# Kernel optimization log

Hardware: AMD Instinct MI355X
Metric: run time of the kernel (lower is better)

## Reference

```python
import jax, jax.numpy as jnp
import numpy as np

B, S, D = 8, 1024, 2048          # batch, seq_len, model dim (q_features == kv_features)
H, HD = 16, 128                   # num_heads, head_dim; H*HD == hidden == 2048


def setup_inputs() -> dict:
    key = jax.random.key(0)
    ks = jax.random.split(key, 6)
    fan_in = 1.0 / np.sqrt(D)     # variance_scaling(1.0, 'fan_in') style init scale
    return {
        "inputs_q": jax.random.normal(ks[0], (B, S, D), jnp.float32),
        "inputs_kv": jax.random.normal(ks[1], (B, S, D), jnp.float32),
        "Wq": jax.random.normal(ks[2], (D, H * HD), jnp.float32) * fan_in,
        "Wk": jax.random.normal(ks[3], (D, H * HD), jnp.float32) * fan_in,
        "Wv": jax.random.normal(ks[4], (D, H * HD), jnp.float32) * fan_in,
        "Wo": jax.random.normal(ks[5], (H * HD, D), jnp.float32) * (1.0 / np.sqrt(H * HD)),
    }


def reference(inputs_q, inputs_kv, Wq, Wk, Wv, Wo):
    b, sq, _ = inputs_q.shape
    skv = inputs_kv.shape[1]
    # QKV projections (DenseGeneral, no bias), reshape to heads
    # scale_attn_logits=True -> query scaled by 1/sqrt(head_dim)
    q = (inputs_q @ Wq).reshape(b, sq, H, HD) * (1.0 / np.sqrt(HD))
    k = (inputs_kv @ Wk).reshape(b, skv, H, HD)
    v = (inputs_kv @ Wv).reshape(b, skv, H, HD)
    # dot-product attention core: [b, h, q, k] scores -> softmax -> context
    scores = jnp.einsum('bqhd,bkhd->bhqk', q, k)
    attn = jax.nn.softmax(scores, axis=-1)
    ctx = jnp.einsum('bhqk,bkhd->bqhd', attn, v).reshape(b, sq, H * HD)
    # output projection back to q_features
    return ctx @ Wo
```

## Files before the change

kernel.cpp:

```cpp
#include <hip/hip_runtime.h>
#include <cstdint>
#include <cstddef>

#define B_  8
#define S_  1024
#define D_  2048
#define H_  16
#define HD_ 128
#define NT_ (D_ / 64)

typedef __bf16 bf16x8 __attribute__((ext_vector_type(8)));
typedef float  f32x4  __attribute__((ext_vector_type(4)));

__device__ __forceinline__ unsigned short f2b(float f) {
    unsigned int u = __float_as_uint(f);
    unsigned int r = (u + 0x7fffu + ((u >> 16) & 1u)) >> 16;
    return (unsigned short)r;
}

__device__ __forceinline__ void gl2lds16(const void* g, void* l) {
    __builtin_amdgcn_global_load_lds(
        (const __attribute__((address_space(1))) void*)g,
        (__attribute__((address_space(3))) void*)l, 16, 0, 0);
}

__global__ void cvt_f32_bf16(const float* __restrict__ src,
                             unsigned short* __restrict__ dst, int n4) {
    int i = blockIdx.x * blockDim.x + threadIdx.x;
    if (i >= n4) return;
    float4 v = ((const float4*)src)[i];
    ushort4 o;
    o.x = f2b(v.x); o.y = f2b(v.y); o.z = f2b(v.z); o.w = f2b(v.w);
    ((ushort4*)dst)[i] = o;
}

__global__ void wtrans(const float* __restrict__ W, unsigned short* __restrict__ Wt) {
    __shared__ float tile[32][33];
    int bx = blockIdx.x, by = blockIdx.y;
    int tx = threadIdx.x, ty = threadIdx.y;
#pragma unroll
    for (int i = 0; i < 4; i++)
        tile[ty + i * 8][tx] = W[(size_t)(by * 32 + ty + i * 8) * D_ + bx * 32 + tx];
    __syncthreads();
#pragma unroll
    for (int i = 0; i < 4; i++)
        Wt[(size_t)(bx * 32 + ty + i * 8) * D_ + by * 32 + tx] = f2b(tile[tx][ty + i * 8]);
}

__global__ void vtrans(const unsigned short* __restrict__ V, unsigned short* __restrict__ Vt) {
    __shared__ unsigned short tile[32][33];
    int bh = blockIdx.z;
    int b = bh >> 4, h = bh & 15;
    int tx = threadIdx.x, ty = threadIdx.y;
    int s0 = blockIdx.x * 32, hd0 = blockIdx.y * 32;
#pragma unroll
    for (int i = 0; i < 4; i++)
        tile[ty + i * 8][tx] = V[(size_t)(b * S_ + s0 + ty + i * 8) * D_ + h * HD_ + hd0 + tx];
    __syncthreads();
#pragma unroll
    for (int i = 0; i < 4; i++)
        Vt[((size_t)bh * HD_ + hd0 + ty + i * 8) * S_ + s0 + tx] = tile[tx][ty + i * 8];
}

#define STAGE1(TN, KH, SRC, DST) do {                                              \
    const int _kb = (TN) * 64 + (KH) * 32;                                         \
    _Pragma("unroll")                                                              \
    for (int _p = 0; _p < 2; _p++) {                                               \
        int _c = _p * 512 + tid;                                                   \
        int _row = _c >> 2;                                                        \
        int _j = (_c & 3) ^ ((_row >> 1) & 3);                                     \
        gl2lds16(SRC + (size_t)_row * D_ + _kb + _j * 8, DST + _c * 8);            \
    }                                                                              \
} while (0)

#define PHASE(SAP, SBP, MH, READB, TN, KH2, SSRC, SDST, VM) do {                   \
    asm volatile("" ::: "memory");                                                 \
    if (READB) {                                                                   \
        _Pragma("unroll")                                                          \
        for (int j = 0; j < 4; j++)                                                \
            bF[j] = *(const bf16x8*)(SAP##_unused, &SBP[(wn + j * 16 + l15) * 32 + swz]); \
    }                                                                              \
    bf16x8 aF[4];                                                                  \
    _Pragma("unroll")                                                              \
    for (int i = 0; i < 4; i++)                                                    \
        aF[i] = *(const bf16x8*)(&SAP[(wm + (MH) * 64 + i * 16 + l15) * 32 + swz]);\
    STAGE1(TN, KH2, SSRC, SDST);                                                   \
    asm volatile("" ::: "memory");                                                 \
    __builtin_amdgcn_s_barrier();                                                  \
    asm volatile("s_waitcnt lgkmcnt(0)" ::: "memory");                             \
    __builtin_amdgcn_sched_barrier(0);                                             \
    __builtin_amdgcn_s_setprio(1);                                                 \
    _Pragma("unroll")                                                              \
    for (int i = 0; i < 4; i++)                                                    \
        _Pragma("unroll")                                                          \
        for (int j = 0; j < 4; j++)                                                \
            acc[(MH) * 4 + i][j] =                                                 \
                __builtin_amdgcn_mfma_f32_16x16x32_bf16(aF[i], bF[j],              \
                                                        acc[(MH) * 4 + i][j], 0, 0, 0); \
    __builtin_amdgcn_s_setprio(0);                                                 \
    if (VM) asm volatile("s_waitcnt vmcnt(4)" ::: "memory");                       \
    asm volatile("" ::: "memory");                                                 \
    __builtin_amdgcn_s_barrier();                                                  \
} while (0)

#define sA00_unused 0
#define sA01_unused 0
#define sA10_unused 0
#define sA11_unused 0

template <bool OUTF>
__global__ void __launch_bounds__(512, 2)
gemm_bt3(const unsigned short* __restrict__ A0, const unsigned short* __restrict__ A1,
         const unsigned short* __restrict__ A2,
         const unsigned short* __restrict__ B0, const unsigned short* __restrict__ B1,
         const unsigned short* __restrict__ B2,
         unsigned short* __restrict__ o0, unsigned short* __restrict__ o1,
         unsigned short* __restrict__ o2, float* __restrict__ oF,
         float s0, float s1, float s2) {
    __shared__ __align__(16) unsigned short sA00[256 * 32], sA01[256 * 32];
    __shared__ __align__(16) unsigned short sA10[256 * 32], sA11[256 * 32];
    __shared__ __align__(16) unsigned short sB00[256 * 32], sB01[256 * 32];
    __shared__ __align__(16) unsigned short sB10[256 * 32], sB11[256 * 32];

    const int tid = threadIdx.x;
    const int w = tid >> 6, lane = tid & 63;
    const int l15 = lane & 15, lhi = lane >> 4;

    const int nwgx = gridDim.x;
    const int nwg = nwgx * gridDim.y;
    const int lin = blockIdx.y * nwgx + blockIdx.x;
    const int per = nwg >> 3;
    const int sw = (lin & 7) * per + (lin >> 3);
    const int bx = sw % nwgx, by = sw / nwgx;

    const int region = bx >> 3;
    const unsigned short* A  = region == 0 ? A0 : (region == 1 ? A1 : A2);
    const unsigned short* Bt = region == 0 ? B0 : (region == 1 ? B1 : B2);
    unsigned short* outB     = region == 0 ? o0 : (region == 1 ? o1 : o2);
    const float scale        = region == 0 ? s0 : (region == 1 ? s1 : s2);
    const int mBase = by * 256;
    const int nBase = (bx & 7) * 256;
    const int wm = (w >> 2) * 128, wn = (w & 3) * 64;

    const unsigned short* Ap = A  + (size_t)mBase * D_;
    const unsigned short* Bp = Bt + (size_t)nBase * D_;

    const int swz = (lhi ^ ((l15 >> 1) & 3)) * 8;

    f32x4 acc[8][4] = {};
    bf16x8 bF[4];

    STAGE1(0, 0, Ap, sA00);
    STAGE1(0, 0, Bp, sB00);
    STAGE1(0, 1, Ap, sA01);
    STAGE1(0, 1, Bp, sB01);
    asm volatile("s_waitcnt vmcnt(4)" ::: "memory");
    asm volatile("" ::: "memory");
    __builtin_amdgcn_s_barrier();

#pragma unroll 1
    for (int tt = 0; tt < NT_; tt += 2) {
        const int t1 = tt + 1;
        const int t2 = (tt + 2) & (NT_ - 1);
        PHASE(sA00, sB00, 0, true , t1, 0, Ap, sA10, false);
        PHASE(sA00, sB00, 1, false, t1, 0, Bp, sB10, true );
        PHASE(sA01, sB01, 0, true , t1, 1, Ap, sA11, false);
        PHASE(sA01, sB01, 1, false, t1, 1, Bp, sB11, true );
        PHASE(sA10, sB10, 0, true , t2, 0, Ap, sA00, false);
        PHASE(sA10, sB10, 1, false, t2, 0, Bp, sB00, true );
        PHASE(sA11, sB11, 0, true , t2, 1, Ap, sA01, false);
        PHASE(sA11, sB11, 1, false, t2, 1, Bp, sB01, true );
    }

#pragma unroll
    for (int ai = 0; ai < 8; ai++) {
#pragma unroll
        for (int j = 0; j < 4; j++) {
#pragma unroll
            for (int r = 0; r < 4; r++) {
                int row = mBase + wm + ai * 16 + lhi * 4 + r;
                int col = nBase + wn + j * 16 + l15;
                float v = acc[ai][j][r] * scale;
                if (OUTF) oF[(size_t)row * D_ + col] = v;
                else      outB[(size_t)row * D_ + col] = f2b(v);
            }
        }
    }
}

#define PSTR 72
__global__ void __launch_bounds__(256, 2)
attn(const unsigned short* __restrict__ Q,
     const unsigned short* __restrict__ Kb,
     const unsigned short* __restrict__ Vt,
     unsigned short* __restrict__ ctx) {
    __shared__ unsigned short sK[64 * 128];
    __shared__ unsigned short sV[128 * 64];
    __shared__ unsigned short sP[4 * 32 * PSTR];
    const int tid = threadIdx.x;
    const int w = tid >> 6, lane = tid & 63;
    const int l15 = lane & 15, lhi = lane >> 4;
    const int qt = blockIdx.x, h = blockIdx.y, b = blockIdx.z;
    const unsigned short* Qp = Q  + (size_t)b * S_ * D_ + h * HD_;
    const unsigned short* Kp = Kb + (size_t)b * S_ * D_ + h * HD_;
    const unsigned short* Vp = Vt + (size_t)(b * H_ + h) * HD_ * S_;
    const int q0 = qt * 128 + w * 32;

    int xoff[2];
#pragma unroll
    for (int ks = 0; ks < 2; ks++)
        xoff[ks] = (((ks * 4 + lhi) ^ (l15 & 7)) * 8);

    bf16x8 qF[2][4];
#pragma unroll
    for (int i = 0; i < 2; i++)
#pragma unroll
        for (int kk = 0; kk < 4; kk++)
            qF[i][kk] = *(const bf16x8*)(Qp + (size_t)(q0 + i * 16 + l15) * D_ + kk * 32 + lhi * 8);

    f32x4 o4[2][8] = {};
    float lrun[2][4] = {};
    unsigned short* sPw = sP + w * 32 * PSTR;

    for (int kt = 0; kt < S_ / 64; kt++) {
        __syncthreads();
#pragma unroll
        for (int p = 0; p < 4; p++) {
            int c = p * 256 + tid;
            {
                int row = c >> 4, pc = c & 15;
                int j = pc ^ (row & 7);
                gl2lds16(Kp + (size_t)(kt * 64 + row) * D_ + j * 8, sK + c * 8);
            }
            {
                int row = c >> 3, pc = c & 7;
                int j = pc ^ (row & 7);
                gl2lds16(Vp + (size_t)row * S_ + kt * 64 + j * 8, sV + c * 8);
            }
        }
        __syncthreads();

        f32x4 s4[2][4] = {};
#pragma unroll
        for (int j = 0; j < 4; j++) {
#pragma unroll
            for (int kk = 0; kk < 4; kk++) {
                bf16x8 bFk = *(const bf16x8*)(sK + (j * 16 + l15) * 128 + ((kk * 4 + lhi) ^ (l15 & 7)) * 8);
#pragma unroll
                for (int i = 0; i < 2; i++)
                    s4[i][j] = __builtin_amdgcn_mfma_f32_16x16x32_bf16(qF[i][kk], bFk, s4[i][j], 0, 0, 0);
            }
        }

#pragma unroll
        for (int i = 0; i < 2; i++) {
#pragma unroll
            for (int r = 0; r < 4; r++) {
                int prow = i * 16 + lhi * 4 + r;
                float ps = 0.f;
#pragma unroll
                for (int j = 0; j < 4; j++) {
                    float pv = exp2f(s4[i][j][r]);
                    ps += pv;
                    sPw[prow * PSTR + j * 16 + l15] = f2b(pv);
                }
                lrun[i][r] += ps;
            }
        }

#pragma unroll
        for (int k2 = 0; k2 < 2; k2++) {
            bf16x8 pF[2];
#pragma unroll
            for (int i = 0; i < 2; i++)
                pF[i] = *(const bf16x8*)(sPw + (i * 16 + l15) * PSTR + k2 * 32 + lhi * 8);
#pragma unroll
            for (int nt = 0; nt < 8; nt++) {
                bf16x8 vF = *(const bf16x8*)(sV + (nt * 16 + l15) * 64 + xoff[k2]);
#pragma unroll
                for (int i = 0; i < 2; i++)
                    o4[i][nt] = __builtin_amdgcn_mfma_f32_16x16x32_bf16(pF[i], vF, o4[i][nt], 0, 0, 0);
            }
        }
    }

#pragma unroll
    for (int i = 0; i < 2; i++)
#pragma unroll
        for (int r = 0; r < 4; r++) {
            float s = lrun[i][r];
#pragma unroll
            for (int msk = 1; msk < 16; msk <<= 1) s += __shfl_xor(s, msk);
            lrun[i][r] = 1.0f / s;
        }
#pragma unroll
    for (int i = 0; i < 2; i++)
#pragma unroll
        for (int nt = 0; nt < 8; nt++)
#pragma unroll
            for (int r = 0; r < 4; r++) {
                size_t row = (size_t)b * S_ + q0 + i * 16 + lhi * 4 + r;
                ctx[row * D_ + h * HD_ + nt * 16 + l15] = f2b(o4[i][nt][r] * lrun[i][r]);
            }
}

extern "C" void kernel_launch(void* const* d_in, const int* in_sizes, int n_in,
                              void* d_out, int out_size, void* d_ws, size_t ws_size,
                              hipStream_t stream) {
    const float* Xq  = (const float*)d_in[0];
    const float* Xkv = (const float*)d_in[1];
    const float* Wq  = (const float*)d_in[2];
    const float* Wk  = (const float*)d_in[3];
    const float* Wv  = (const float*)d_in[4];
    const float* Wo  = (const float*)d_in[5];
    float* out = (float*)d_out;

    char* ws = (char*)d_ws;
    const size_t XSZ = (size_t)B_ * S_ * D_ * 2;
    const size_t WSZ = (size_t)D_ * D_ * 2;
    unsigned short* XqB  = (unsigned short*)(ws);
    unsigned short* XkvB = (unsigned short*)(ws + XSZ);
    unsigned short* WqT  = (unsigned short*)(ws + 2 * XSZ);
    unsigned short* WkT  = (unsigned short*)(ws + 2 * XSZ + WSZ);
    unsigned short* WvT  = (unsigned short*)(ws + 2 * XSZ + 2 * WSZ);
    unsigned short* WoT  = (unsigned short*)(ws + 2 * XSZ + 3 * WSZ);
    unsigned short* Qb   = (unsigned short*)(ws + 3 * XSZ);
    unsigned short* Kb   = (unsigned short*)(ws + 4 * XSZ);
    unsigned short* Vb   = (unsigned short*)(ws + 5 * XSZ);
    unsigned short* VtB  = XkvB;
    unsigned short* ctxB = XqB;

    const int n4 = B_ * S_ * D_ / 4;
    cvt_f32_bf16<<<n4 / 256, 256, 0, stream>>>(Xq,  XqB,  n4);
    cvt_f32_bf16<<<n4 / 256, 256, 0, stream>>>(Xkv, XkvB, n4);

    dim3 tb(32, 8);
    wtrans<<<dim3(64, 64), tb, 0, stream>>>(Wq, WqT);
    wtrans<<<dim3(64, 64), tb, 0, stream>>>(Wk, WkT);
    wtrans<<<dim3(64, 64), tb, 0, stream>>>(Wv, WvT);
    wtrans<<<dim3(64, 64), tb, 0, stream>>>(Wo, WoT);

    const float qscale = 1.44269504088896f / 11.313708498984761f;

    gemm_bt3<false><<<dim3(24, 32), 512, 0, stream>>>(
        XqB, XkvB, XkvB, WqT, WkT, WvT, Qb, Kb, Vb, nullptr, qscale, 1.0f, 1.0f);

    vtrans<<<dim3(S_ / 32, HD_ / 32, B_ * H_), tb, 0, stream>>>(Vb, VtB);

    attn<<<dim3(S_ / 128, H_, B_), 256, 0, stream>>>(Qb, Kb, VtB, ctxB);

    gemm_bt3<true><<<dim3(8, 32), 512, 0, stream>>>(
        ctxB, ctxB, ctxB, WoT, WoT, WoT, nullptr, nullptr, nullptr, out, 1.0f, 1.0f, 1.0f);
}
```

Before: 638.0 us.

## Restructure GEMM mainloop as four-stage ring of 32-wide K tiles

Measured after the change: 639.4 us. Within noise of the previous version (+0.2%).

```diff
diff --git a/kernel.cpp b/kernel.cpp
--- a/kernel.cpp
+++ b/kernel.cpp
@@ -7,7 +7,7 @@
 #define D_  2048
 #define H_  16
 #define HD_ 128
-#define NT_ (D_ / 64)
+#define NT32_ 64
 
 typedef __bf16 bf16x8 __attribute__((ext_vector_type(8)));
 typedef float  f32x4  __attribute__((ext_vector_type(4)));
@@ -62,65 +62,67 @@
         Vt[((size_t)bh * HD_ + hd0 + ty + i * 8) * S_ + s0 + tx] = tile[tx][ty + i * 8];
 }
 
-#define STAGE1(TN, KH, SRC, DST) do {                                              \
-    const int _kb = (TN) * 64 + (KH) * 32;                                         \
+#define STAGE(TS, SRC, DST) do {                                                   \
+    const int _kb = (TS) * 32;                                                     \
     _Pragma("unroll")                                                              \
     for (int _p = 0; _p < 2; _p++) {                                               \
         int _c = _p * 512 + tid;                                                   \
         int _row = _c >> 2;                                                        \
-        int _j = (_c & 3) ^ ((_row >> 1) & 3);                                     \
+        int _j = (_c & 3) ^ (_row & 3);                                            \
         gl2lds16(SRC + (size_t)_row * D_ + _kb + _j * 8, DST + _c * 8);            \
     }                                                                              \
 } while (0)
 
-#define PHASE(SAP, SBP, MH, READB, TN, KH2, SSRC, SDST, VM) do {                   \
-    asm volatile("" ::: "memory");                                                 \
-    if (READB) {                                                                   \
-        _Pragma("unroll")                                                          \
-        for (int j = 0; j < 4; j++)                                                \
-            bF[j] = *(const bf16x8*)(SAP##_unused, &SBP[(wn + j * 16 + l15) * 32 + swz]); \
-    }                                                                              \
-    bf16x8 aF[4];                                                                  \
+#define GTILE(SA, SB, SDA, SDB, TS) do {                                           \
+    bf16x8 bF[4], aF[4];                                                           \
+    _Pragma("unroll")                                                              \
+    for (int j = 0; j < 4; j++)                                                    \
+        bF[j] = *(const bf16x8*)(SB + (wn + j * 16 + l15) * 32 + swz);             \
     _Pragma("unroll")                                                              \
     for (int i = 0; i < 4; i++)                                                    \
-        aF[i] = *(const bf16x8*)(&SAP[(wm + (MH) * 64 + i * 16 + l15) * 32 + swz]);\
-    STAGE1(TN, KH2, SSRC, SDST);                                                   \
-    asm volatile("" ::: "memory");                                                 \
+        aF[i] = *(const bf16x8*)(SA + (wm + i * 16 + l15) * 32 + swz);             \
+    STAGE(TS, Ap, SDA);                                                            \
     __builtin_amdgcn_s_barrier();                                                  \
-    asm volatile("s_waitcnt lgkmcnt(0)" ::: "memory");                             \
-    __builtin_amdgcn_sched_barrier(0);                                             \
     __builtin_amdgcn_s_setprio(1);                                                 \
     _Pragma("unroll")                                                              \
     for (int i = 0; i < 4; i++)                                                    \
         _Pragma("unroll")                                                          \
         for (int j = 0; j < 4; j++)                                                \
-            acc[(MH) * 4 + i][j] =                                                 \
-                __builtin_amdgcn_mfma_f32_16x16x32_bf16(aF[i], bF[j],              \
-                                                        acc[(MH) * 4 + i][j], 0, 0, 0); \
+            acc[i][j] = __builtin_amdgcn_mfma_f32_16x16x32_bf16(aF[i], bF[j],      \
+                                                               acc[i][j], 0, 0, 0); \
     __builtin_amdgcn_s_setprio(0);                                                 \
-    if (VM) asm volatile("s_waitcnt vmcnt(4)" ::: "memory");                       \
-    asm volatile("" ::: "memory");                                                 \
+    __builtin_amdgcn_s_barrier();                                                  \
+    _Pragma("unroll")                                                              \
+    for (int i = 0; i < 4; i++)                                                    \
+        aF[i] = *(const bf16x8*)(SA + (wm + 64 + i * 16 + l15) * 32 + swz);        \
+    STAGE(TS, Bp, SDB);                                                            \
+    __builtin_amdgcn_s_barrier();                                                  \
+    __builtin_amdgcn_s_setprio(1);                                                 \
+    _Pragma("unroll")                                                              \
+    for (int i = 0; i < 4; i++)                                                    \
+        _Pragma("unroll")                                                          \
+        for (int j = 0; j < 4; j++)                                                \
+            acc[4 + i][j] = __builtin_amdgcn_mfma_f32_16x16x32_bf16(aF[i], bF[j],  \
+                                                               acc[4 + i][j], 0, 0, 0); \
+    __builtin_amdgcn_s_setprio(0);                                                 \
+    asm volatile("s_waitcnt vmcnt(8)");                                            \
+    __builtin_amdgcn_sched_barrier(0);                                             \
     __builtin_amdgcn_s_barrier();                                                  \
 } while (0)
 
-#define sA00_unused 0
-#define sA01_unused 0
-#define sA10_unused 0
-#define sA11_unused 0
-
 template <bool OUTF>
 __global__ void __launch_bounds__(512, 2)
-gemm_bt3(const unsigned short* __restrict__ A0, const unsigned short* __restrict__ A1,
+gemm_bt4(const unsigned short* __restrict__ A0, const unsigned short* __restrict__ A1,
          const unsigned short* __restrict__ A2,
          const unsigned short* __restrict__ B0, const unsigned short* __restrict__ B1,
          const unsigned short* __restrict__ B2,
          unsigned short* __restrict__ o0, unsigned short* __restrict__ o1,
          unsigned short* __restrict__ o2, float* __restrict__ oF,
          float s0, float s1, float s2) {
-    __shared__ __align__(16) unsigned short sA00[256 * 32], sA01[256 * 32];
-    __shared__ __align__(16) unsigned short sA10[256 * 32], sA11[256 * 32];
-    __shared__ __align__(16) unsigned short sB00[256 * 32], sB01[256 * 32];
-    __shared__ __align__(16) unsigned short sB10[256 * 32], sB11[256 * 32];
+    __shared__ __align__(16) unsigned short sA0[256 * 32], sA1[256 * 32];
+    __shared__ __align__(16) unsigned short sA2[256 * 32], sA3[256 * 32];
+    __shared__ __align__(16) unsigned short sB0[256 * 32], sB1[256 * 32];
+    __shared__ __align__(16) unsigned short sB2[256 * 32], sB3[256 * 32];
 
     const int tid = threadIdx.x;
     const int w = tid >> 6, lane = tid & 63;
@@ -145,32 +147,28 @@
     const unsigned short* Ap = A  + (size_t)mBase * D_;
     const unsigned short* Bp = Bt + (size_t)nBase * D_;
 
-    const int swz = (lhi ^ ((l15 >> 1) & 3)) * 8;
+    const int swz = (lhi ^ (l15 & 3)) * 8;
 
     f32x4 acc[8][4] = {};
-    bf16x8 bF[4];
-
-    STAGE1(0, 0, Ap, sA00);
-    STAGE1(0, 0, Bp, sB00);
-    STAGE1(0, 1, Ap, sA01);
-    STAGE1(0, 1, Bp, sB01);
-    asm volatile("s_waitcnt vmcnt(4)" ::: "memory");
-    asm volatile("" ::: "memory");
+
+    STAGE(0, Ap, sA0); STAGE(0, Bp, sB0);
+    STAGE(1, Ap, sA1); STAGE(1, Bp, sB1);
+    STAGE(2, Ap, sA2); STAGE(2, Bp, sB2);
+    asm volatile("s_waitcnt vmcnt(8)");
+    __builtin_amdgcn_sched_barrier(0);
     __builtin_amdgcn_s_barrier();
 
 #pragma unroll 1
-    for (int tt = 0; tt < NT_; tt += 2) {
-        const int t1 = tt + 1;
-        const int t2 = (tt + 2) & (NT_ - 1);
-        PHASE(sA00, sB00, 0, true , t1, 0, Ap, sA10, false);
-        PHASE(sA00, sB00, 1, false, t1, 0, Bp, sB10, true );
-        PHASE(sA01, sB01, 0, true , t1, 1, Ap, sA11, false);
-        PHASE(sA01, sB01, 1, false, t1, 1, Bp, sB11, true );
-        PHASE(sA10, sB10, 0, true , t2, 0, Ap, sA00, false);
-        PHASE(sA10, sB10, 1, false, t2, 0, Bp, sB00, true );
-        PHASE(sA11, sB11, 0, true , t2, 1, Ap, sA01, false);
-        PHASE(sA11, sB11, 1, false, t2, 1, Bp, sB01, true );
+    for (int tt = 0; tt < NT32_; tt += 4) {
+        GTILE(sA0, sB0, sA3, sB3, (tt + 3) & (NT32_ - 1));
+        GTILE(sA1, sB1, sA0, sB0, (tt + 4) & (NT32_ - 1));
+        GTILE(sA2, sB2, sA1, sB1, (tt + 5) & (NT32_ - 1));
+        GTILE(sA3, sB3, sA2, sB2, (tt + 6) & (NT32_ - 1));
     }
+
+    asm volatile("s_waitcnt vmcnt(0)");
+    __builtin_amdgcn_sched_barrier(0);
+    __builtin_amdgcn_s_barrier();
 
 #pragma unroll
     for (int ai = 0; ai < 8; ai++) {
@@ -342,13 +340,13 @@
 
     const float qscale = 1.44269504088896f / 11.313708498984761f;
 
-    gemm_bt3<false><<<dim3(24, 32), 512, 0, stream>>>(
+    gemm_bt4<false><<<dim3(24, 32), 512, 0, stream>>>(
         XqB, XkvB, XkvB, WqT, WkT, WvT, Qb, Kb, Vb, nullptr, qscale, 1.0f, 1.0f);
 
     vtrans<<<dim3(S_ / 32, HD_ / 32, B_ * H_), tb, 0, stream>>>(Vb, VtB);
 
     attn<<<dim3(S_ / 128, H_, B_), 256, 0, stream>>>(Qb, Kb, VtB, ctxB);
 
-    gemm_bt3<true><<<dim3(8, 32), 512, 0, stream>>>(
+    gemm_bt4<true><<<dim3(8, 32), 512, 0, stream>>>(
         ctxB, ctxB, ctxB, WoT, WoT, WoT, nullptr, nullptr, nullptr, out, 1.0f, 1.0f, 1.0f);
 }
```
